# Kernel optimization log

Hardware: AMD Instinct MI355X
Metric: run time of the kernel (lower is better)

The kernel has to match this reference:

```python
import jax, jax.numpy as jnp
import numpy as np

B, T, E, H, D, NL = 2, 1024, 2048, 16, 128, 3
MAXL = T * (2 ** (NL - 1))  # k length doubles each layer: T, 2T, 4T


def _rms_norm(x, w, eps=1e-5):
    return x * jax.lax.rsqrt(jnp.mean(x * x, axis=-1, keepdims=True) + eps) * w


def _rope(x, cos, sin):
    # x: [B, S, H, D]; cos/sin: [>=S, D/2]; GPT-NeoX style (non-interleaved)
    S = x.shape[1]
    c = cos[:S][None, :, None, :]
    s = sin[:S][None, :, None, :]
    x1, x2 = jnp.split(x, 2, axis=-1)
    return jnp.concatenate([x1 * c - x2 * s, x1 * s + x2 * c], axis=-1)


def _causal_attn(q, k, v):
    # bottom-right-aligned causal (flash_attn_func causal=True with kv longer than q)
    Tq, L = q.shape[1], k.shape[1]
    scale = 1.0 / np.sqrt(q.shape[-1]).astype(np.float32)
    scores = jnp.einsum('bthd,bshd->bhts', q, k) * scale
    i = jnp.arange(Tq)[:, None]
    j = jnp.arange(L)[None, :]
    mask = j <= i + (L - Tq)
    scores = jnp.where(mask[None, None], scores, -jnp.inf)
    p = jax.nn.softmax(scores, axis=-1)
    return jnp.einsum('bhts,bshd->bthd', p, v)


def setup_inputs() -> dict:
    key = jax.random.key(0)
    ks = jax.random.split(key, 6)
    x = jax.random.normal(ks[0], (B, T, E), dtype=jnp.float32)
    inv_freq = 1.0 / (10000.0 ** (np.arange(0, D, 2, dtype=np.float32) / D))  # [D/2]
    ang = np.arange(MAXL, dtype=np.float32)[:, None] * inv_freq[None, :]      # [MAXL, D/2]
    cos = jnp.asarray(np.cos(ang), dtype=jnp.float32)
    sin = jnp.asarray(np.sin(ang), dtype=jnp.float32)
    wq = jax.random.normal(ks[1], (NL, E, E), dtype=jnp.float32) * 0.02
    wk = jax.random.normal(ks[2], (NL, E, E), dtype=jnp.float32) * 0.02
    wv = jax.random.normal(ks[3], (NL, E, E), dtype=jnp.float32) * 0.02
    ln_w = jnp.ones((NL, E), dtype=jnp.float32)
    lambdas = jnp.zeros((NL,), dtype=jnp.float32)
    w_out = jax.random.normal(ks[4], (E, E), dtype=jnp.float32) * 0.02
    final_ln_w = jnp.ones((E,), dtype=jnp.float32)
    alpha = jnp.ones((1,), dtype=jnp.float32)
    return {'x': x, 'cos': cos, 'sin': sin, 'wq': wq, 'wk': wk, 'wv': wv,
            'ln_w': ln_w, 'lambdas': lambdas, 'w_out': w_out,
            'final_ln_w': final_ln_w, 'alpha': alpha}


def reference(x, cos, sin, wq, wk, wv, ln_w, lambdas, w_out, final_ln_w, alpha):
    bsz, tgt_len, embed_dim = x.shape
    # lambda weights: sigmoid then LayerNorm over the NL scalars (no affine)
    lam = jax.nn.sigmoid(lambdas)
    lam = (lam - jnp.mean(lam)) * jax.lax.rsqrt(jnp.var(lam) + 1e-5)
    acc_k, acc_v = [], []
    total = jnp.zeros_like(x)
    for i in range(NL):  # small fixed layer count
        q = (x @ wq[i].T).reshape(bsz, tgt_len, H, D)
        k = (x @ wk[i].T).reshape(bsz, tgt_len, H, D)
        v = (x @ wv[i].T).reshape(bsz, tgt_len, H, D)
        if i > 0:
            k = jnp.concatenate([k] + acc_k, axis=1)
            v = jnp.concatenate([v] + acc_v, axis=1)
        q = _rope(q, cos, sin)
        k = _rope(k, cos, sin)  # note: cached K gets rotary re-applied, as in source
        attn = _causal_attn(q, k, v).reshape(bsz, tgt_len, embed_dim)
        attn = _rms_norm(attn, ln_w[i])
        total = total + attn * lam[i]
        acc_k.append(k)
        acc_v.append(v)
    out = _rms_norm(total + alpha * x, final_ln_w)
    return out @ w_out.T
```

## Files before the change

### kernel.cpp

```cpp
#include <hip/hip_runtime.h>
#include <hip/hip_bf16.h>

typedef unsigned short ushort_t;
typedef __attribute__((ext_vector_type(8))) short bf16x8;
typedef __attribute__((ext_vector_type(4))) short bf16x4;
typedef __attribute__((ext_vector_type(4))) float f32x4;
typedef __attribute__((ext_vector_type(4))) unsigned short u16x4;
typedef __attribute__((ext_vector_type(4))) unsigned int u32x4;

#define DEV __device__ __forceinline__

DEV ushort_t f2bf(float f) {
  __hip_bfloat16 h = __float2bfloat16(f);
  return __builtin_bit_cast(unsigned short, h);
}
DEV float bf2f(ushort_t b) {
  union { float f; unsigned int u; } a; a.u = ((unsigned int)b) << 16;
  return a.f;
}
DEV void gload_lds16(const void* g, void* l) {
  __builtin_amdgcn_global_load_lds((const __attribute__((address_space(1))) void*)g,
                                   (__attribute__((address_space(3))) void*)l, 16, 0, 0);
}
DEV unsigned ldsaddr(const void* l) {
  return (unsigned)(unsigned long long)(const __attribute__((address_space(3))) void*)l;
}
template <int OFF>
DEV bf16x4 tr16o(unsigned a) {
  bf16x4 d;
  asm volatile("ds_read_b64_tr_b16 %0, %1 offset:%c2" : "=v"(d) : "v"(a), "i"(OFF));
  return d;
}
template <int OFF>
DEV bf16x8 ldsb128o(unsigned a) {
  bf16x8 d;
  asm volatile("ds_read_b128 %0, %1 offset:%c2" : "=v"(d) : "v"(a), "i"(OFF));
  return d;
}

__global__ __launch_bounds__(256) void f2b_kernel(const float* __restrict__ in,
                                                  ushort_t* __restrict__ out, int n) {
  int base = (blockIdx.x * 256 + threadIdx.x) * 4;
  if (base >= n) return;
  f32x4 v = *(const f32x4*)(in + base);
  u16x4 o;
  o.x = f2bf(v.x); o.y = f2bf(v.y); o.z = f2bf(v.z); o.w = f2bf(v.w);
  *(u16x4*)(out + base) = o;
}

__global__ __launch_bounds__(256) void f2b3_kernel(const float* __restrict__ a, const float* __restrict__ b,
                                                   const float* __restrict__ c, ushort_t* __restrict__ out) {
  int id = blockIdx.x * 256 + threadIdx.x;
  int sel = id >> 20, k = (id & 1048575) * 4;
  const float* src = sel == 0 ? a : sel == 1 ? b : c;
  f32x4 v = *(const f32x4*)(src + k);
  u16x4 o;
  o.x = f2bf(v.x); o.y = f2bf(v.y); o.z = f2bf(v.z); o.w = f2bf(v.w);
  *(u16x4*)(out + (size_t)sel * 4194304 + k) = o;
}

__global__ void lam_kernel(const float* __restrict__ lambdas, float* __restrict__ lam) {
  if (threadIdx.x == 0 && blockIdx.x == 0) {
    float l0 = 1.f / (1.f + __expf(-lambdas[0]));
    float l1 = 1.f / (1.f + __expf(-lambdas[1]));
    float l2 = 1.f / (1.f + __expf(-lambdas[2]));
    float mean = (l0 + l1 + l2) * (1.f / 3.f);
    float d0 = l0 - mean, d1 = l1 - mean, d2 = l2 - mean;
    float var = (d0 * d0 + d1 * d1 + d2 * d2) * (1.f / 3.f);
    float rs = rsqrtf(var + 1e-5f);
    lam[0] = d0 * rs; lam[1] = d1 * rs; lam[2] = d2 * rs;
  }
}

DEV void gemm_core(const ushort_t* __restrict__ A, const ushort_t* __restrict__ Bm,
                   ushort_t* lsA, ushort_t* lsB, int bm, int bn, int kbeg, int kend,
                   f32x4 (&acc)[4][4]) {
  const int K = 2048;
  int tid = threadIdx.x;
  int w = tid >> 6, lane = tid & 63;
  int g = lane >> 4, r = lane & 15;
  int wm = w >> 1, wn = w & 1;
#pragma unroll
  for (int i = 0; i < 4; ++i)
#pragma unroll
    for (int j = 0; j < 4; ++j) acc[i][j] = 0.f;

  for (int kk = kbeg; kk < kend; kk += 32) {
    __syncthreads();
#pragma unroll
    for (int j2 = 0; j2 < 2; ++j2) {
      int eb = w * 1024 + j2 * 512;
      int ebl = eb + lane * 8;
      int rr = ebl >> 5, cc = ebl & 31;
      gload_lds16(A + (size_t)(bm * 128 + rr) * K + kk + cc, lsA + eb);
      gload_lds16(Bm + (size_t)(bn * 128 + rr) * K + kk + cc, lsB + eb);
    }
    __syncthreads();
    bf16x8 af[4], bfr[4];
#pragma unroll
    for (int i = 0; i < 4; ++i)
      af[i] = *(const bf16x8*)(lsA + (wm * 64 + i * 16 + r) * 32 + g * 8);
#pragma unroll
    for (int j = 0; j < 4; ++j)
      bfr[j] = *(const bf16x8*)(lsB + (wn * 64 + j * 16 + r) * 32 + g * 8);
#pragma unroll
    for (int i = 0; i < 4; ++i)
#pragma unroll
      for (int j = 0; j < 4; ++j)
        acc[i][j] = __builtin_amdgcn_mfma_f32_16x16x32_bf16(af[i], bfr[j], acc[i][j], 0, 0, 0);
  }
}

#define MM(i, j)                                                                              \
  acc[i][j] = __builtin_amdgcn_mfma_f32_16x16x32_bf16(af[(i) & 3][0], bfr[j][0], acc[i][j], 0, 0, 0); \
  acc[i][j] = __builtin_amdgcn_mfma_f32_16x16x32_bf16(af[(i) & 3][1], bfr[j][1], acc[i][j], 0, 0, 0);

__global__ __launch_bounds__(512, 2) void gemm_qkv256(
    const ushort_t* __restrict__ A,
    const ushort_t* __restrict__ Bq, const ushort_t* __restrict__ Bk, const ushort_t* __restrict__ Bv,
    ushort_t* __restrict__ Cq, ushort_t* __restrict__ Ck, ushort_t* __restrict__ Cv, int Lkv) {
  __shared__ __align__(16) ushort_t lsA[32768];
  __shared__ __align__(16) ushort_t lsB[32768];
  const int NT = 32;

  int bid = (int)blockIdx.x;
  int swz = (bid & 7) * 24 + (bid >> 3);
  int bm = swz / 24;
  int rest = swz % 24;
  int sel = rest >> 3, bnc = rest & 7;
  const ushort_t* Bmat = (sel == 0) ? Bq : (sel == 1) ? Bk : Bv;
  ushort_t* C = (sel == 0) ? Cq : (sel == 1) ? Ck : Cv;
  int Lsel = (sel == 0) ? 1024 : Lkv;

  int tid = threadIdx.x;
  int wv = tid >> 6, lane = tid & 63;
  int wm = wv >> 2, wn = wv & 3;
  int g = lane >> 4, r = lane & 15;

  int row0 = tid >> 3, c0 = tid & 7;
  int colsw = (c0 ^ (row0 & 7)) * 8;
  const ushort_t* pA0 = A + (size_t)(bm * 256 + row0) * 2048 + colsw;
  const ushort_t* pB0 = Bmat + (size_t)(bnc * 256 + row0) * 2048 + colsw;
  ushort_t* dA = lsA + tid * 8;
  ushort_t* dB = lsB + tid * 8;

  auto SA = [&](int T, int hh) {
    const ushort_t* s = pA0 + (size_t)(hh * 128) * 2048 + (size_t)T * 64;
    ushort_t* d = dA + (T & 1) * 16384 + hh * 8192;
    gload_lds16(s, d);
    gload_lds16(s + (size_t)64 * 2048, d + 4096);
  };
  auto SB = [&](int T, int hh) {
    const ushort_t* s = pB0 + (size_t)(hh * 128) * 2048 + (size_t)T * 64;
    ushort_t* d = dB + (T & 1) * 16384 + hh * 8192;
    gload_lds16(s, d);
    gload_lds16(s + (size_t)64 * 2048, d + 4096);
  };

  unsigned xm = (unsigned)(r & 7);
  unsigned aAb = ldsaddr(lsA) + (unsigned)((wm * 128 + r) * 128);
  unsigned aA0b = aAb + ((((unsigned)g) ^ xm) << 4);
  unsigned aA1b = aAb + ((((unsigned)(4 + g)) ^ xm) << 4);
  unsigned aBb = ldsaddr(lsB) + (unsigned)((wn * 64 + r) * 128);
  unsigned aB0b = aBb + ((((unsigned)g) ^ xm) << 4);
  unsigned aB1b = aBb + ((((unsigned)(4 + g)) ^ xm) << 4);

  f32x4 acc[8][4];
#pragma unroll
  for (int i = 0; i < 8; ++i)
#pragma unroll
    for (int j = 0; j < 4; ++j) acc[i][j] = 0.f;
  bf16x8 af[4][2], bfr[4][2];

  SA(0, 0); SB(0, 0); SB(0, 1); SA(0, 1);
  SA(1, 0); SB(1, 0); SB(1, 1);
  asm volatile("s_waitcnt vmcnt(6)" ::: "memory");
  __builtin_amdgcn_s_barrier();
  __builtin_amdgcn_sched_barrier(0);

  for (int t = 0; t < NT; ++t) {
    unsigned cb = (unsigned)((t & 1) << 15);
    unsigned A0 = aA0b + cb, A1 = aA1b + cb, B0 = aB0b + cb, B1 = aB1b + cb;
    bool full = (t < NT - 2);
    af[0][0] = ldsb128o<0>(A0);     af[0][1] = ldsb128o<0>(A1);
    af[1][0] = ldsb128o<2048>(A0);  af[1][1] = ldsb128o<2048>(A1);
    af[2][0] = ldsb128o<4096>(A0);  af[2][1] = ldsb128o<4096>(A1);
    af[3][0] = ldsb128o<6144>(A0);  af[3][1] = ldsb128o<6144>(A1);
    bfr[0][0] = ldsb128o<0>(B0);    bfr[0][1] = ldsb128o<0>(B1);
    bfr[1][0] = ldsb128o<2048>(B0); bfr[1][1] = ldsb128o<2048>(B1);
    if (t + 1 < NT) SA(t + 1, 1);
    __builtin_amdgcn_s_barrier();
    asm volatile("s_waitcnt lgkmcnt(0)" ::: "memory");
    __builtin_amdgcn_sched_barrier(0);
    __builtin_amdgcn_s_setprio(1);
    MM(0, 0) MM(1, 0) MM(2, 0) MM(3, 0) MM(0, 1) MM(1, 1) MM(2, 1) MM(3, 1)
    __builtin_amdgcn_s_setprio(0);
    __builtin_amdgcn_sched_barrier(0);
    __builtin_amdgcn_s_barrier();
    bfr[2][0] = ldsb128o<4096>(B0); bfr[2][1] = ldsb128o<4096>(B1);
    bfr[3][0] = ldsb128o<6144>(B0); bfr[3][1] = ldsb128o<6144>(B1);
    if (full) SA(t + 2, 0);
    __builtin_amdgcn_s_barrier();
    asm volatile("s_waitcnt lgkmcnt(0)" ::: "memory");
    __builtin_amdgcn_sched_barrier(0);
    __builtin_amdgcn_s_setprio(1);
    MM(0, 2) MM(1, 2) MM(2, 2) MM(3, 2) MM(0, 3) MM(1, 3) MM(2, 3) MM(3, 3)
    __builtin_amdgcn_s_setprio(0);
    if (full) { asm volatile("s_waitcnt vmcnt(4)" ::: "memory"); }
    else      { asm volatile("s_waitcnt vmcnt(0)" ::: "memory"); }
    __builtin_amdgcn_sched_barrier(0);
    __builtin_amdgcn_s_barrier();
    af[0][0] = ldsb128o<8192>(A0);  af[0][1] = ldsb128o<8192>(A1);
    af[1][0] = ldsb128o<10240>(A0); af[1][1] = ldsb128o<10240>(A1);
    af[2][0] = ldsb128o<12288>(A0); af[2][1] = ldsb128o<12288>(A1);
    af[3][0] = ldsb128o<14336>(A0); af[3][1] = ldsb128o<14336>(A1);
    if (full) SB(t + 2, 0);
    __builtin_amdgcn_s_barrier();
    asm volatile("s_waitcnt lgkmcnt(0)" ::: "memory");
    __builtin_amdgcn_sched_barrier(0);
    __builtin_amdgcn_s_setprio(1);
    MM(4, 2) MM(5, 2) MM(6, 2) MM(7, 2) MM(4, 3) MM(5, 3) MM(6, 3) MM(7, 3)
    __builtin_amdgcn_s_setprio(0);
    __builtin_amdgcn_sched_barrier(0);
    __builtin_amdgcn_s_barrier();
    if (full) SB(t + 2, 1);
    __builtin_amdgcn_s_barrier();
    __builtin_amdgcn_s_setprio(1);
    MM(4, 0) MM(5, 0) MM(6, 0) MM(7, 0) MM(4, 1) MM(5, 1) MM(6, 1) MM(7, 1)
    __builtin_amdgcn_s_setprio(0);
    if (full) { asm volatile("s_waitcnt vmcnt(8)" ::: "memory"); }
    else      { asm volatile("s_waitcnt vmcnt(0)" ::: "memory"); }
    __builtin_amdgcn_sched_barrier(0);
    __builtin_amdgcn_s_barrier();
  }

  int prow = bm * 256 + wm * 128 + g * 4;
  int pcol = bnc * 256 + wn * 64 + r;
#pragma unroll
  for (int i = 0; i < 8; ++i)
#pragma unroll
    for (int j = 0; j < 4; ++j) {
      int col = pcol + j * 16;
#pragma unroll
      for (int tt = 0; tt < 4; ++tt) {
        int row = prow + i * 16 + tt;
        int b2 = row >> 10, t2 = row & 1023;
        C[(size_t)(b2 * Lsel + t2) * 2048 + col] = f2bf(acc[i][j][tt]);
      }
    }
}
#undef MM

__global__ __launch_bounds__(256) void gemm_bt_part(
    const ushort_t* __restrict__ A, const ushort_t* __restrict__ Bm, float* __restrict__ P) {
  __shared__ __align__(16) ushort_t lsA[4096];
  __shared__ __align__(16) ushort_t lsB[4096];
  int bn = blockIdx.x, bm = blockIdx.y, s = blockIdx.z;
  f32x4 acc[4][4];
  gemm_core(A, Bm, lsA, lsB, bm, bn, s * 1024, (s + 1) * 1024, acc);
  float* C = P + (size_t)s * 4194304;
  int lane = threadIdx.x & 63, w = threadIdx.x >> 6;
  int g = lane >> 4, r = lane & 15, wm = w >> 1, wn = w & 1;
#pragma unroll
  for (int i = 0; i < 4; ++i)
#pragma unroll
    for (int j = 0; j < 4; ++j) {
      int row0 = bm * 128 + wm * 64 + i * 16 + g * 4;
      int col = bn * 128 + wn * 64 + j * 16 + r;
#pragma unroll
      for (int t = 0; t < 4; ++t)
        C[(size_t)(row0 + t) * 2048 + col] = acc[i][j][t];
    }
}

__global__ __launch_bounds__(256) void add2_kernel(const float* __restrict__ a, const float* __restrict__ b,
                                                   float* __restrict__ out) {
  int i = (blockIdx.x * 256 + threadIdx.x) * 4;
  f32x4 va = *(const f32x4*)(a + i);
  f32x4 vb = *(const f32x4*)(b + i);
  f32x4 r;
#pragma unroll
  for (int k = 0; k < 4; ++k) r[k] = va[k] + vb[k];
  *(f32x4*)(out + i) = r;
}

DEV void rope_body(const ushort_t* src, ushort_t* dst, const float* cosT, const float* sinT,
                   int Ls, int s0, int Ld, int dpos0, int cnt, int bp) {
  int b = bp / cnt, pidx = bp % cnt;
  int pos = dpos0 + pidx;
  int pi = threadIdx.x * 4;
  int h = pi >> 6, d = pi & 63;
  const ushort_t* s_ = src + ((size_t)(b * Ls + s0 + pidx) * 16 + h) * 128 + d;
  ushort_t* d_ = dst + ((size_t)(b * Ld + pos) * 16 + h) * 128 + d;
  f32x4 c4 = *(const f32x4*)(cosT + (size_t)pos * 64 + d);
  f32x4 s4 = *(const f32x4*)(sinT + (size_t)pos * 64 + d);
  u16x4 x1 = *(const u16x4*)(s_);
  u16x4 x2 = *(const u16x4*)(s_ + 64);
  u16x4 o1, o2;
#pragma unroll
  for (int k = 0; k < 4; ++k) {
    float a = bf2f(x1[k]), bb = bf2f(x2[k]);
    o1[k] = f2bf(a * c4[k] - bb * s4[k]);
    o2[k] = f2bf(a * s4[k] + bb * c4[k]);
  }
  *(u16x4*)d_ = o1;
  *(u16x4*)(d_ + 64) = o2;
}
DEV void copy_body(const ushort_t* src, ushort_t* dst, int Ls, int s0, int Ld, int dpos0,
                   int cnt, int bp) {
  int b = bp / cnt, pidx = bp % cnt;
  const u32x4* s = (const u32x4*)(src + (size_t)(b * Ls + s0 + pidx) * 2048);
  u32x4* d = (u32x4*)(dst + (size_t)(b * Ld + dpos0 + pidx) * 2048);
  d[threadIdx.x] = s[threadIdx.x];
}

__global__ __launch_bounds__(256) void rope_k(ushort_t* Kc, const float* __restrict__ cosT,
                                              const float* __restrict__ sinT, int L) {
  rope_body(Kc, Kc, cosT, sinT, L, 0, L, 0, 1024, blockIdx.x);
}

__global__ __launch_bounds__(256) void layer1_cache(const ushort_t* __restrict__ K0, ushort_t* __restrict__ K1,
                                                    ushort_t* __restrict__ K2,
                                                    const ushort_t* __restrict__ V0, ushort_t* __restrict__ V1,
                                                    const float* __restrict__ cosT, const float* __restrict__ sinT) {
  int bp = blockIdx.x;
  if (bp < 2048) {
    int b = bp >> 10, pidx = bp & 1023;
    int pos = 1024 + pidx;
    int pi = threadIdx.x * 4;
    int h = pi >> 6, d = pi & 63;
    size_t io = ((size_t)h) * 128 + d;
    const ushort_t* s_ = K0 + ((size_t)(b * 1024 + pidx) * 16) * 128 + io;
    ushort_t* d1 = K1 + ((size_t)(b * 2048 + pos) * 16) * 128 + io;
    ushort_t* d2 = K2 + ((size_t)(b * 4096 + pos) * 16) * 128 + io;
    f32x4 c4 = *(const f32x4*)(cosT + (size_t)pos * 64 + d);
    f32x4 s4 = *(const f32x4*)(sinT + (size_t)pos * 64 + d);
    u16x4 x1 = *(const u16x4*)(s_);
    u16x4 x2 = *(const u16x4*)(s_ + 64);
    u16x4 o1, o2;
#pragma unroll
    for (int k = 0; k < 4; ++k) {
      float a = bf2f(x1[k]), bb = bf2f(x2[k]);
      o1[k] = f2bf(a * c4[k] - bb * s4[k]);
      o2[k] = f2bf(a * s4[k] + bb * c4[k]);
    }
    *(u16x4*)d1 = o1;
    *(u16x4*)(d1 + 64) = o2;
    *(u16x4*)d2 = o1;
    *(u16x4*)(d2 + 64) = o2;
  } else {
    copy_body(V0, V1, 1024, 0, 2048, 1024, 1024, bp - 2048);
  }
}

__global__ __launch_bounds__(256) void layer2_cache(const ushort_t* __restrict__ K1, ushort_t* __restrict__ K2,
                                                    const ushort_t* __restrict__ V1, ushort_t* __restrict__ V2,
                                                    const float* __restrict__ cosT, const float* __restrict__ sinT) {
  int bp = blockIdx.x;
  if (bp < 4096) rope_body(K1, K2, cosT, sinT, 2048, 0, 4096, 2048, 2048, bp);
  else if (bp < 6144) copy_body(V1, V2, 2048, 1024, 4096, 1024, 1024, bp - 4096);
  else copy_body(V1, V2, 2048, 0, 4096, 2048, 2048, bp - 6144);
}

__global__ __launch_bounds__(256, 4) void attn_kernel(
    const ushort_t* __restrict__ Qraw, const ushort_t* __restrict__ Kc, const ushort_t* __restrict__ Vc,
    const float* __restrict__ cosT, const float* __restrict__ sinT,
    ushort_t* __restrict__ Opart, float2* __restrict__ Ml, int Lk) {
  __shared__ __align__(16) ushort_t lsK[8192];
  __shared__ __align__(16) ushort_t lsV[8192];
  const float SC2 = 0.1275174366f;

  int bid = (int)blockIdx.x;
  int swz = (bid & 7) * 128 + (bid >> 3);
  int s = swz & 1;
  int rest = swz >> 1;

  int w = threadIdx.x >> 6, lane = threadIdx.x & 63;
  int bq = rest & 15, h = (rest >> 4) & 15, b = rest >> 8;
  int qt = bq * 4 + w;
  int g = lane >> 4, r = lane & 15;
  int off = Lk - 1024;

  const ushort_t* qbase = Qraw + ((size_t)(b * 1024 + qt * 16 + r) * 16 + h) * 128;
  int pos = qt * 16 + r;
  const float* cb = cosT + (size_t)pos * 64;
  const float* sb = sinT + (size_t)pos * 64;
  bf16x8 qf[4];
#pragma unroll
  for (int c = 0; c < 2; ++c) {
    int d0 = c * 32 + g * 8;
    f32x4 c0 = *(const f32x4*)(cb + d0);
    f32x4 c1 = *(const f32x4*)(cb + d0 + 4);
    f32x4 s0 = *(const f32x4*)(sb + d0);
    f32x4 s1 = *(const f32x4*)(sb + d0 + 4);
    bf16x8 x1 = *(const bf16x8*)(qbase + d0);
    bf16x8 x2 = *(const bf16x8*)(qbase + d0 + 64);
    bf16x8 lo, hi;
#pragma unroll
    for (int k = 0; k < 8; ++k) {
      float cv = (k < 4 ? c0[k] : c1[k - 4]) * SC2;
      float sv = (k < 4 ? s0[k] : s1[k - 4]) * SC2;
      float a = bf2f((ushort_t)x1[k]);
      float bb = bf2f((ushort_t)x2[k]);
      lo[k] = (short)f2bf(a * cv - bb * sv);
      hi[k] = (short)f2bf(a * sv + bb * cv);
    }
    qf[c] = lo; qf[c + 2] = hi;
  }

  int t = threadIdx.x;
  int krow0 = t >> 4,        kc0 = (t & 15) ^ (krow0 & 7);
  int krow1 = (t + 256) >> 4, kc1 = (t & 15) ^ (krow1 & 7);
  const size_t adv = 32 * 2048;
  const size_t adv2 = 2 * adv;
  const ushort_t* srcK0 = Kc + ((size_t)(b * Lk + krow0) * 16 + h) * 128 + kc0 * 8 + s * adv;
  const ushort_t* srcK1 = Kc + ((size_t)(b * Lk + krow1) * 16 + h) * 128 + kc1 * 8 + s * adv;
  int L0 = t, L1 = t + 256;
  int vrow0 = ((L0 >> 3) & 7) * 4 + ((L0 >> 1) & 3), vd0 = (L0 >> 6) * 16 + (L0 & 1) * 8;
  int vrow1 = ((L1 >> 3) & 7) * 4 + ((L1 >> 1) & 3), vd1 = (L1 >> 6) * 16 + (L1 & 1) * 8;
  const ushort_t* srcV0 = Vc + ((size_t)(b * Lk + vrow0) * 16 + h) * 128 + vd0 + s * adv;
  const ushort_t* srcV1 = Vc + ((size_t)(b * Lk + vrow1) * 16 + h) * 128 + vd1 + s * adv;

  auto STAGE = [&](int buf) {
    ushort_t* k0 = lsK + buf * 4096 + w * 512;
    ushort_t* v0 = lsV + buf * 4096 + w * 512;
    gload_lds16(srcK0, k0);
    gload_lds16(srcK1, k0 + 2048);
    gload_lds16(srcV0, v0);
    gload_lds16(srcV1, v0 + 2048);
    srcK0 += adv2; srcK1 += adv2; srcV0 += adv2; srcV1 += adv2;
  };

  unsigned kx[4];
  unsigned kbase0 = ldsaddr(lsK) + (unsigned)(r * 256);
#pragma unroll
  for (int c = 0; c < 4; ++c)
    kx[c] = kbase0 + (unsigned)((((c * 32 + g * 8) ^ ((r & 7) * 8))) * 2);
  unsigned vbase0 = ldsaddr(lsV);

  float m_run = -1e30f, l_run = 0.f;
  f32x4 o[8];
#pragma unroll
  for (int c = 0; c < 8; ++c) o[c] = 0.f;

  int qp = qt * 16 + r + off;
  int qmin = qt * 16 + off;
  int nkt_w = ((qt * 16 + 15 + off) >> 5) + 1;
  int nkt_blk = (((bq * 4 + 3) * 16 + 15 + off) >> 5) + 1;
  int ntile = (nkt_blk - s + 1) >> 1;

#define LDK(c, ks) ldsb128o<(ks) * 4096>(kx[c] + kb)
#define LDV(hh, i) tr16o<(hh) * 4096 + (i) * 512>(vb)

  if (ntile > 0) {
    STAGE(0);
    for (int it = 0; it < ntile; ++it) {
      int kt = s + it * 2;
      int cur = it & 1;
      if (it + 1 < ntile) {
        STAGE(cur ^ 1);
        asm volatile("s_waitcnt vmcnt(4)" ::: "memory");
      } else {
        asm volatile("s_waitcnt vmcnt(0)" ::: "memory");
      }
      __builtin_amdgcn_s_barrier();
      __builtin_amdgcn_sched_barrier(0);
      if (kt < nkt_w) {
        unsigned kb = (unsigned)(cur << 13);
        unsigned vb = vbase0 + kb;
        f32x4 st[2];
        {
          bf16x8 k0 = LDK(0, 0), k1 = LDK(1, 0), k2 = LDK(2, 0), k3 = LDK(3, 0);
          asm volatile("s_waitcnt lgkmcnt(0)" ::: "memory");
          __builtin_amdgcn_sched_barrier(0);
          __builtin_amdgcn_s_setprio(1);
          f32x4 acc = 0.f;
          acc = __builtin_amdgcn_mfma_f32_16x16x32_bf16(k0, qf[0], acc, 0, 0, 0);
          acc = __builtin_amdgcn_mfma_f32_16x16x32_bf16(k1, qf[1], acc, 0, 0, 0);
          acc = __builtin_amdgcn_mfma_f32_16x16x32_bf16(k2, qf[2], acc, 0, 0, 0);
          acc = __builtin_amdgcn_mfma_f32_16x16x32_bf16(k3, qf[3], acc, 0, 0, 0);
          __builtin_amdgcn_s_setprio(0);
          st[0] = acc;
        }
        {
          bf16x8 k0 = LDK(0, 1), k1 = LDK(1, 1), k2 = LDK(2, 1), k3 = LDK(3, 1);
          asm volatile("s_waitcnt lgkmcnt(0)" ::: "memory");
          __builtin_amdgcn_sched_barrier(0);
          __builtin_amdgcn_s_setprio(1);
          f32x4 acc = 0.f;
          acc = __builtin_amdgcn_mfma_f32_16x16x32_bf16(k0, qf[0], acc, 0, 0, 0);
          acc = __builtin_amdgcn_mfma_f32_16x16x32_bf16(k1, qf[1], acc, 0, 0, 0);
          acc = __builtin_amdgcn_mfma_f32_16x16x32_bf16(k2, qf[2], acc, 0, 0, 0);
          acc = __builtin_amdgcn_mfma_f32_16x16x32_bf16(k3, qf[3], acc, 0, 0, 0);
          __builtin_amdgcn_s_setprio(0);
          st[1] = acc;
        }
        float pmaxl = -1e30f;
        int kp0 = kt * 32;
        if (kp0 + 31 > qmin) {
#pragma unroll
          for (int ks = 0; ks < 2; ++ks)
#pragma unroll
            for (int j = 0; j < 4; ++j) {
              int key = kp0 + ks * 16 + g * 4 + j;
              float sv = st[ks][j];
              if (key > qp) sv = -1e30f;
              st[ks][j] = sv;
              pmaxl = fmaxf(pmaxl, sv);
            }
        } else {
#pragma unroll
          for (int ks = 0; ks < 2; ++ks)
#pragma unroll
            for (int j = 0; j < 4; ++j) pmaxl = fmaxf(pmaxl, st[ks][j]);
        }
        if (!__all(pmaxl <= m_run + 11.5f)) {
          float pmax = fmaxf(pmaxl, __shfl_xor(pmaxl, 16, 64));
          pmax = fmaxf(pmax, __shfl_xor(pmax, 32, 64));
          if (pmax > m_run + 11.5f) {
            float mnew = fmaxf(m_run, pmax);
            float corr = exp2f(m_run - mnew);
            l_run *= corr;
#pragma unroll
            for (int c = 0; c < 8; ++c)
#pragma unroll
              for (int tt = 0; tt < 4; ++tt) o[c][tt] *= corr;
            m_run = mnew;
          }
        }
        float psum = 0.f;
        bf16x4 pf[2];
#pragma unroll
        for (int ks = 0; ks < 2; ++ks)
#pragma unroll
          for (int j = 0; j < 4; ++j) {
            float pe = exp2f(st[ks][j] - m_run);
            psum += pe;
            pf[ks][j] = (short)f2bf(pe);
          }
        psum += __shfl_xor(psum, 16, 64);
        psum += __shfl_xor(psum, 32, 64);
        l_run += psum;
        {
          bf16x4 v0 = LDV(0, 0), v1 = LDV(0, 1), v2 = LDV(0, 2), v3 = LDV(0, 3);
          bf16x4 v4 = LDV(0, 4), v5 = LDV(0, 5), v6 = LDV(0, 6), v7 = LDV(0, 7);
          asm volatile("s_waitcnt lgkmcnt(0)" ::: "memory");
          __builtin_amdgcn_sched_barrier(0);
          __builtin_amdgcn_s_setprio(1);
          o[0] = __builtin_amdgcn_mfma_f32_16x16x16bf16_1k(v0, pf[0], o[0], 0, 0, 0);
          o[0] = __builtin_amdgcn_mfma_f32_16x16x16bf16_1k(v1, pf[1], o[0], 0, 0, 0);
          o[1] = __builtin_amdgcn_mfma_f32_16x16x16bf16_1k(v2, pf[0], o[1], 0, 0, 0);
          o[1] = __builtin_amdgcn_mfma_f32_16x16x16bf16_1k(v3, pf[1], o[1], 0, 0, 0);
          o[2] = __builtin_amdgcn_mfma_f32_16x16x16bf16_1k(v4, pf[0], o[2], 0, 0, 0);
          o[2] = __builtin_amdgcn_mfma_f32_16x16x16bf16_1k(v5, pf[1], o[2], 0, 0, 0);
          o[3] = __builtin_amdgcn_mfma_f32_16x16x16bf16_1k(v6, pf[0], o[3], 0, 0, 0);
          o[3] = __builtin_amdgcn_mfma_f32_16x16x16bf16_1k(v7, pf[1], o[3], 0, 0, 0);
          __builtin_amdgcn_s_setprio(0);
        }
        {
          bf16x4 v0 = LDV(1, 0), v1 = LDV(1, 1), v2 = LDV(1, 2), v3 = LDV(1, 3);
          bf16x4 v4 = LDV(1, 4), v5 = LDV(1, 5), v6 = LDV(1, 6), v7 = LDV(1, 7);
          asm volatile("s_waitcnt lgkmcnt(0)" ::: "memory");
          __builtin_amdgcn_sched_barrier(0);
          __builtin_amdgcn_s_setprio(1);
          o[4] = __builtin_amdgcn_mfma_f32_16x16x16bf16_1k(v0, pf[0], o[4], 0, 0, 0);
          o[4] = __builtin_amdgcn_mfma_f32_16x16x16bf16_1k(v1, pf[1], o[4], 0, 0, 0);
          o[5] = __builtin_amdgcn_mfma_f32_16x16x16bf16_1k(v2, pf[0], o[5], 0, 0, 0);
          o[5] = __builtin_amdgcn_mfma_f32_16x16x16bf16_1k(v3, pf[1], o[5], 0, 0, 0);
          o[6] = __builtin_amdgcn_mfma_f32_16x16x16bf16_1k(v4, pf[0], o[6], 0, 0, 0);
          o[6] = __builtin_amdgcn_mfma_f32_16x16x16bf16_1k(v5, pf[1], o[6], 0, 0, 0);
          o[7] = __builtin_amdgcn_mfma_f32_16x16x16bf16_1k(v6, pf[0], o[7], 0, 0, 0);
          o[7] = __builtin_amdgcn_mfma_f32_16x16x16bf16_1k(v7, pf[1], o[7], 0, 0, 0);
          __builtin_amdgcn_s_setprio(0);
        }
      }
      __builtin_amdgcn_sched_barrier(0);
      __builtin_amdgcn_s_barrier();
    }
  }
#undef LDK
#undef LDV
  ushort_t* ob = Opart + (size_t)s * 4194304 + ((size_t)(b * 1024 + qt * 16 + r) * 16 + h) * 128;
#pragma unroll
  for (int dblk = 0; dblk < 8; ++dblk) {
    u16x4 ov;
#pragma unroll
    for (int tt = 0; tt < 4; ++tt) ov[tt] = f2bf(o[dblk][tt]);
    *(u16x4*)(ob + dblk * 16 + g * 4) = ov;
  }
  if (g == 0) {
    float2 ml; ml.x = m_run; ml.y = l_run;
    Ml[((size_t)(s * 2 + b) * 1024 + qt * 16 + r) * 16 + h] = ml;
  }
}

template <int FIRST>
__global__ __launch_bounds__(256) void rms_combine(const ushort_t* __restrict__ Opart, const float2* __restrict__ Ml,
                                                   const float* __restrict__ lnw, const float* __restrict__ lam,
                                                   int li, float* __restrict__ total) {
  int row = blockIdx.x;
  int t8 = threadIdx.x * 8;
  int h = t8 >> 7;
  float2 ml0 = Ml[(size_t)row * 16 + h];
  float2 ml1 = Ml[(size_t)(row + 2048) * 16 + h];
  float M = fmaxf(ml0.x, ml1.x);
  float w0 = exp2f(ml0.x - M), w1 = exp2f(ml1.x - M);
  float rinv = 1.f / (w0 * ml0.y + w1 * ml1.y);
  w0 *= rinv; w1 *= rinv;
  const ushort_t* a0 = Opart + (size_t)row * 2048 + t8;
  const ushort_t* a1 = a0 + 4194304;
  u16x4 p00 = *(const u16x4*)(a0);
  u16x4 p01 = *(const u16x4*)(a0 + 4);
  u16x4 p10 = *(const u16x4*)(a1);
  u16x4 p11 = *(const u16x4*)(a1 + 4);
  f32x4 v0, v1;
#pragma unroll
  for (int k = 0; k < 4; ++k) {
    v0[k] = w0 * bf2f(p00[k]) + w1 * bf2f(p10[k]);
    v1[k] = w0 * bf2f(p01[k]) + w1 * bf2f(p11[k]);
  }
  float ss = v0.x * v0.x + v0.y * v0.y + v0.z * v0.z + v0.w * v0.w +
             v1.x * v1.x + v1.y * v1.y + v1.z * v1.z + v1.w * v1.w;
#pragma unroll
  for (int m = 1; m < 64; m <<= 1) ss += __shfl_xor(ss, m, 64);
  __shared__ float red[4];
  int w = threadIdx.x >> 6, lane = threadIdx.x & 63;
  if (lane == 0) red[w] = ss;
  __syncthreads();
  ss = red[0] + red[1] + red[2] + red[3];
  float sca = rsqrtf(ss * (1.f / 2048.f) + 1e-5f) * lam[li];
  f32x4 w0v = *(const f32x4*)(lnw + t8);
  f32x4 w1v = *(const f32x4*)(lnw + t8 + 4);
  float* o = total + (size_t)row * 2048 + t8;
  f32x4 r0, r1;
#pragma unroll
  for (int k = 0; k < 4; ++k) { r0[k] = v0[k] * sca * w0v[k]; r1[k] = v1[k] * sca * w1v[k]; }
  if (!FIRST) {
    f32x4 q0 = *(const f32x4*)(o);
    f32x4 q1 = *(const f32x4*)(o + 4);
#pragma unroll
    for (int k = 0; k < 4; ++k) { r0[k] += q0[k]; r1[k] += q1[k]; }
  }
  *(f32x4*)(o) = r0;
  *(f32x4*)(o + 4) = r1;
}

__global__ __launch_bounds__(256) void final_norm(const float* __restrict__ total, const float* __restrict__ x,
                                                  const float* __restrict__ alphap, const float* __restrict__ flw,
                                                  ushort_t* __restrict__ ybf) {
  int row = blockIdx.x;
  float al = alphap[0];
  int t8 = threadIdx.x * 8;
  const float* tp = total + (size_t)row * 2048 + t8;
  const float* xp = x + (size_t)row * 2048 + t8;
  f32x4 t0 = *(const f32x4*)(tp);
  f32x4 t1 = *(const f32x4*)(tp + 4);
  f32x4 x0 = *(const f32x4*)(xp);
  f32x4 x1 = *(const f32x4*)(xp + 4);
  float y[8];
#pragma unroll
  for (int k = 0; k < 4; ++k) { y[k] = t0[k] + al * x0[k]; y[4 + k] = t1[k] + al * x1[k]; }
  float ss = 0.f;
#pragma unroll
  for (int k = 0; k < 8; ++k) ss += y[k] * y[k];
#pragma unroll
  for (int m = 1; m < 64; m <<= 1) ss += __shfl_xor(ss, m, 64);
  __shared__ float red[4];
  int w = threadIdx.x >> 6, lane = threadIdx.x & 63;
  if (lane == 0) red[w] = ss;
  __syncthreads();
  ss = red[0] + red[1] + red[2] + red[3];
  float s = rsqrtf(ss * (1.f / 2048.f) + 1e-5f);
  f32x4 w0 = *(const f32x4*)(flw + t8);
  f32x4 w1 = *(const f32x4*)(flw + t8 + 4);
  u16x4 o0, o1;
#pragma unroll
  for (int k = 0; k < 4; ++k) {
    o0[k] = f2bf(y[k] * s * w0[k]);
    o1[k] = f2bf(y[4 + k] * s * w1[k]);
  }
  *(u16x4*)(ybf + (size_t)row * 2048 + t8) = o0;
  *(u16x4*)(ybf + (size_t)row * 2048 + t8 + 4) = o1;
}

extern "C" void kernel_launch(void* const* d_in, const int* in_sizes, int n_in,
                              void* d_out, int out_size, void* d_ws, size_t ws_size,
                              hipStream_t stream) {
  const float* x = (const float*)d_in[0];
  const float* cosT = (const float*)d_in[1];
  const float* sinT = (const float*)d_in[2];
  const float* wq = (const float*)d_in[3];
  const float* wk = (const float*)d_in[4];
  const float* wv = (const float*)d_in[5];
  const float* lnw = (const float*)d_in[6];
  const float* lambdas = (const float*)d_in[7];
  const float* w_out = (const float*)d_in[8];
  const float* flw = (const float*)d_in[9];
  const float* alpha = (const float*)d_in[10];

  const size_t ME = 4194304ull;
  char* p = (char*)d_ws;
  size_t off = 0;
  auto alc = [&](size_t bytes) -> void* {
    void* r = p + off;
    off += (bytes + 255) & ~(size_t)255;
    return r;
  };
  ushort_t* xb = (ushort_t*)alc(ME * 2);
  void* uni = alc(2 * ME * 4);
  ushort_t* wl = (ushort_t*)uni;
  ushort_t* Opart = (ushort_t*)uni;
  float* Ppart = (float*)uni;
  ushort_t* q = (ushort_t*)alc(ME * 2);
  ushort_t* K0 = (ushort_t*)alc(ME * 2);
  ushort_t* K1 = (ushort_t*)alc(2 * ME * 2);
  ushort_t* K2 = (ushort_t*)alc(4 * ME * 2);
  ushort_t* V0 = (ushort_t*)alc(ME * 2);
  ushort_t* V1 = (ushort_t*)alc(2 * ME * 2);
  ushort_t* V2 = (ushort_t*)alc(4 * ME * 2);
  float* total = (float*)alc(ME * 4);
  float2* Ml = (float2*)alc(65536 * 8);
  float* lam = (float*)alc(256);
  ushort_t* ybf = q;
  ushort_t* wob = K0;

  f2b_kernel<<<4096, 256, 0, stream>>>(x, xb, 4194304);
  lam_kernel<<<1, 64, 0, stream>>>(lambdas, lam);

  ushort_t* Kc[3] = {K0, K1, K2};
  ushort_t* Vc[3] = {V0, V1, V2};

  for (int li = 0; li < 3; ++li) {
    int L = 1024 << li;
    size_t woff = (size_t)li * ME;
    f2b3_kernel<<<12288, 256, 0, stream>>>(wq + woff, wk + woff, wv + woff, wl);
    gemm_qkv256<<<192, 512, 0, stream>>>(xb, wl, wl + ME, wl + 2 * ME,
                                         q, Kc[li], Vc[li], L);
    rope_k<<<2048, 256, 0, stream>>>(Kc[li], cosT, sinT, L);
    if (li == 1)
      layer1_cache<<<4096, 256, 0, stream>>>(K0, K1, K2, V0, V1, cosT, sinT);
    else if (li == 2)
      layer2_cache<<<10240, 256, 0, stream>>>(K1, K2, V1, V2, cosT, sinT);
    attn_kernel<<<1024, 256, 0, stream>>>(q, Kc[li], Vc[li], cosT, sinT, Opart, Ml, L);
    if (li == 0)
      rms_combine<1><<<2048, 256, 0, stream>>>(Opart, Ml, lnw, lam, 0, total);
    else
      rms_combine<0><<<2048, 256, 0, stream>>>(Opart, Ml, lnw + (size_t)li * 2048, lam, li, total);
  }

  f2b_kernel<<<4096, 256, 0, stream>>>(w_out, wob, 4194304);
  final_norm<<<2048, 256, 0, stream>>>(total, x, alpha, flw, ybf);
  gemm_bt_part<<<dim3(16, 16, 2), 256, 0, stream>>>(ybf, wob, Ppart);
  add2_kernel<<<4096, 256, 0, stream>>>(Ppart, Ppart + ME, (float*)d_out);
}
```

Measured before the change: 542.6 us.

## Fuse final RMS norm into last-layer combine and use split-K 4 for output GEMM

Merges the final norm (residual add with alpha*x and final RMSNorm to bf16) into the layer-2 attention combine kernel, avoiding a separate launch and a write/read of the fp32 total buffer. The output projection GEMM is split over four K chunks instead of two, with partials stored in the now-free V2 cache buffer and summed by a four-way add kernel. This raises parallelism for the final GEMM at the cost of extra partial-sum traffic and a longer reduction.

```diff
diff --git a/kernel.cpp b/kernel.cpp
--- a/kernel.cpp
+++ b/kernel.cpp
@@ -251,14 +251,15 @@
 }
 #undef MM
 
-__global__ __launch_bounds__(256) void gemm_bt_part(
-    const ushort_t* __restrict__ A, const ushort_t* __restrict__ Bm, float* __restrict__ P) {
+__global__ __launch_bounds__(256, 4) void gemm_bt_part(
+    const ushort_t* __restrict__ A, const ushort_t* __restrict__ Bm,
+    float* __restrict__ P01, float* __restrict__ P23) {
   __shared__ __align__(16) ushort_t lsA[4096];
   __shared__ __align__(16) ushort_t lsB[4096];
   int bn = blockIdx.x, bm = blockIdx.y, s = blockIdx.z;
   f32x4 acc[4][4];
-  gemm_core(A, Bm, lsA, lsB, bm, bn, s * 1024, (s + 1) * 1024, acc);
-  float* C = P + (size_t)s * 4194304;
+  gemm_core(A, Bm, lsA, lsB, bm, bn, s * 512, (s + 1) * 512, acc);
+  float* C = (s < 2 ? P01 + (size_t)s * 4194304 : P23 + (size_t)(s - 2) * 4194304);
   int lane = threadIdx.x & 63, w = threadIdx.x >> 6;
   int g = lane >> 4, r = lane & 15, wm = w >> 1, wn = w & 1;
 #pragma unroll
@@ -273,14 +274,17 @@
     }
 }
 
-__global__ __launch_bounds__(256) void add2_kernel(const float* __restrict__ a, const float* __restrict__ b,
+__global__ __launch_bounds__(256) void add4_kernel(const float* __restrict__ a, const float* __restrict__ b,
+                                                   const float* __restrict__ c, const float* __restrict__ d,
                                                    float* __restrict__ out) {
   int i = (blockIdx.x * 256 + threadIdx.x) * 4;
   f32x4 va = *(const f32x4*)(a + i);
   f32x4 vb = *(const f32x4*)(b + i);
+  f32x4 vc = *(const f32x4*)(c + i);
+  f32x4 vd = *(const f32x4*)(d + i);
   f32x4 r;
 #pragma unroll
-  for (int k = 0; k < 4; ++k) r[k] = va[k] + vb[k];
+  for (int k = 0; k < 4; ++k) r[k] = (va[k] + vb[k]) + (vc[k] + vd[k]);
   *(f32x4*)(out + i) = r;
 }
 
@@ -645,24 +649,35 @@
   *(f32x4*)(o + 4) = r1;
 }
 
-__global__ __launch_bounds__(256) void final_norm(const float* __restrict__ total, const float* __restrict__ x,
-                                                  const float* __restrict__ alphap, const float* __restrict__ flw,
-                                                  ushort_t* __restrict__ ybf) {
+__global__ __launch_bounds__(256) void rms_combine_final(
+    const ushort_t* __restrict__ Opart, const float2* __restrict__ Ml,
+    const float* __restrict__ lnw, const float* __restrict__ lam,
+    const float* __restrict__ total, const float* __restrict__ x,
+    const float* __restrict__ alphap, const float* __restrict__ flw,
+    ushort_t* __restrict__ ybf) {
   int row = blockIdx.x;
-  float al = alphap[0];
   int t8 = threadIdx.x * 8;
-  const float* tp = total + (size_t)row * 2048 + t8;
-  const float* xp = x + (size_t)row * 2048 + t8;
-  f32x4 t0 = *(const f32x4*)(tp);
-  f32x4 t1 = *(const f32x4*)(tp + 4);
-  f32x4 x0 = *(const f32x4*)(xp);
-  f32x4 x1 = *(const f32x4*)(xp + 4);
-  float y[8];
-#pragma unroll
-  for (int k = 0; k < 4; ++k) { y[k] = t0[k] + al * x0[k]; y[4 + k] = t1[k] + al * x1[k]; }
-  float ss = 0.f;
-#pragma unroll
-  for (int k = 0; k < 8; ++k) ss += y[k] * y[k];
+  int h = t8 >> 7;
+  float2 ml0 = Ml[(size_t)row * 16 + h];
+  float2 ml1 = Ml[(size_t)(row + 2048) * 16 + h];
+  float M = fmaxf(ml0.x, ml1.x);
+  float w0 = exp2f(ml0.x - M), w1 = exp2f(ml1.x - M);
+  float rinv = 1.f / (w0 * ml0.y + w1 * ml1.y);
+  w0 *= rinv; w1 *= rinv;
+  const ushort_t* a0 = Opart + (size_t)row * 2048 + t8;
+  const ushort_t* a1 = a0 + 4194304;
+  u16x4 p00 = *(const u16x4*)(a0);
+  u16x4 p01 = *(const u16x4*)(a0 + 4);
+  u16x4 p10 = *(const u16x4*)(a1);
+  u16x4 p11 = *(const u16x4*)(a1 + 4);
+  f32x4 v0, v1;
+#pragma unroll
+  for (int k = 0; k < 4; ++k) {
+    v0[k] = w0 * bf2f(p00[k]) + w1 * bf2f(p10[k]);
+    v1[k] = w0 * bf2f(p01[k]) + w1 * bf2f(p11[k]);
+  }
+  float ss = v0.x * v0.x + v0.y * v0.y + v0.z * v0.z + v0.w * v0.w +
+             v1.x * v1.x + v1.y * v1.y + v1.z * v1.z + v1.w * v1.w;
 #pragma unroll
   for (int m = 1; m < 64; m <<= 1) ss += __shfl_xor(ss, m, 64);
   __shared__ float red[4];
@@ -670,14 +685,39 @@
   if (lane == 0) red[w] = ss;
   __syncthreads();
   ss = red[0] + red[1] + red[2] + red[3];
-  float s = rsqrtf(ss * (1.f / 2048.f) + 1e-5f);
-  f32x4 w0 = *(const f32x4*)(flw + t8);
-  f32x4 w1 = *(const f32x4*)(flw + t8 + 4);
+  float sca = rsqrtf(ss * (1.f / 2048.f) + 1e-5f) * lam[2];
+  f32x4 w0v = *(const f32x4*)(lnw + t8);
+  f32x4 w1v = *(const f32x4*)(lnw + t8 + 4);
+  const float* tp = total + (size_t)row * 2048 + t8;
+  const float* xp = x + (size_t)row * 2048 + t8;
+  f32x4 q0 = *(const f32x4*)(tp);
+  f32x4 q1 = *(const f32x4*)(tp + 4);
+  f32x4 x0 = *(const f32x4*)(xp);
+  f32x4 x1 = *(const f32x4*)(xp + 4);
+  float al = alphap[0];
+  float y[8];
+#pragma unroll
+  for (int k = 0; k < 4; ++k) {
+    y[k]     = q0[k] + v0[k] * sca * w0v[k] + al * x0[k];
+    y[4 + k] = q1[k] + v1[k] * sca * w1v[k] + al * x1[k];
+  }
+  float ss2 = 0.f;
+#pragma unroll
+  for (int k = 0; k < 8; ++k) ss2 += y[k] * y[k];
+#pragma unroll
+  for (int m = 1; m < 64; m <<= 1) ss2 += __shfl_xor(ss2, m, 64);
+  __syncthreads();
+  if (lane == 0) red[w] = ss2;
+  __syncthreads();
+  ss2 = red[0] + red[1] + red[2] + red[3];
+  float s2 = rsqrtf(ss2 * (1.f / 2048.f) + 1e-5f);
+  f32x4 f0 = *(const f32x4*)(flw + t8);
+  f32x4 f1 = *(const f32x4*)(flw + t8 + 4);
   u16x4 o0, o1;
 #pragma unroll
   for (int k = 0; k < 4; ++k) {
-    o0[k] = f2bf(y[k] * s * w0[k]);
-    o1[k] = f2bf(y[4 + k] * s * w1[k]);
+    o0[k] = f2bf(y[k] * s2 * f0[k]);
+    o1[k] = f2bf(y[4 + k] * s2 * f1[k]);
   }
   *(u16x4*)(ybf + (size_t)row * 2048 + t8) = o0;
   *(u16x4*)(ybf + (size_t)row * 2048 + t8 + 4) = o1;
@@ -710,7 +750,7 @@
   void* uni = alc(2 * ME * 4);
   ushort_t* wl = (ushort_t*)uni;
   ushort_t* Opart = (ushort_t*)uni;
-  float* Ppart = (float*)uni;
+  float* Ppart01 = (float*)uni;
   ushort_t* q = (ushort_t*)alc(ME * 2);
   ushort_t* K0 = (ushort_t*)alc(ME * 2);
   ushort_t* K1 = (ushort_t*)alc(2 * ME * 2);
@@ -723,6 +763,7 @@
   float* lam = (float*)alc(256);
   ushort_t* ybf = q;
   ushort_t* wob = K0;
+  float* Ppart23 = (float*)V2;
 
   f2b_kernel<<<4096, 256, 0, stream>>>(x, xb, 4194304);
   lam_kernel<<<1, 64, 0, stream>>>(lambdas, lam);
@@ -744,12 +785,14 @@
     attn_kernel<<<1024, 256, 0, stream>>>(q, Kc[li], Vc[li], cosT, sinT, Opart, Ml, L);
     if (li == 0)
       rms_combine<1><<<2048, 256, 0, stream>>>(Opart, Ml, lnw, lam, 0, total);
+    else if (li == 1)
+      rms_combine<0><<<2048, 256, 0, stream>>>(Opart, Ml, lnw + (size_t)2048, lam, 1, total);
     else
-      rms_combine<0><<<2048, 256, 0, stream>>>(Opart, Ml, lnw + (size_t)li * 2048, lam, li, total);
+      rms_combine_final<<<2048, 256, 0, stream>>>(Opart, Ml, lnw + (size_t)2 * 2048, lam,
+                                                  total, x, alpha, flw, ybf);
   }
 
   f2b_kernel<<<4096, 256, 0, stream>>>(w_out, wob, 4194304);
-  final_norm<<<2048, 256, 0, stream>>>(total, x, alpha, flw, ybf);
-  gemm_bt_part<<<dim3(16, 16, 2), 256, 0, stream>>>(ybf, wob, Ppart);
-  add2_kernel<<<4096, 256, 0, stream>>>(Ppart, Ppart + ME, (float*)d_out);
-}
+  gemm_bt_part<<<dim3(16, 16, 4), 256, 0, stream>>>(ybf, wob, Ppart01, Ppart23);
+  add4_kernel<<<4096, 256, 0, stream>>>(Ppart01, Ppart01 + ME, Ppart23, Ppart23 + ME, (float*)d_out);
+}
```

Result: no change. 544.4 us (+0.3%).
